# Kernel optimization log

Measured on AMD Instinct MI355X. Metric: run time of the kernel, lower is better.

The kernel has to match this reference:

```python
import jax, jax.numpy as jnp
import numpy as np

N_DIMS = 4          # len(dims): gauge-link channels split off by unpack_x
N_BANDS = 3         # SU(3) matrices
THRESHOLD = 1e-3    # trnorm_threshold
LAYER_CH = [6, 12, 12]  # input_channels + args.layer_channels


def cplx_einsum(eq, a, b):
    # complex einsum on real/imag-stacked tensors (last dim = 2)
    ar, ai = a[..., 0], a[..., 1]
    br, bi = b[..., 0], b[..., 1]
    re = jnp.einsum(eq, ar, br) - jnp.einsum(eq, ai, bi)
    im = jnp.einsum(eq, ar, bi) + jnp.einsum(eq, ai, br)
    return jnp.stack((re, im), axis=-1)


def h_conj(w):
    # hermitian conjugate: transpose matrix dims, negate imag part
    wt = jnp.swapaxes(w, -3, -2)
    return jnp.stack((wt[..., 0], -wt[..., 1]), axis=-1)


def gebl(x, weight):
    # x: [b, X, n_dims + n_in, nb, nb, 2]; weight: [n_out, w_in, w_in, 2]
    u, w = x[:, :, :N_DIMS], x[:, :, N_DIMS:]
    w = jnp.concatenate((w, h_conj(w)), axis=2)            # conjugation enlargement
    b, s = w.shape[0], w.shape[1]
    eye = jnp.zeros((N_BANDS, N_BANDS, 2), w.dtype).at[..., 0].set(jnp.eye(N_BANDS, dtype=w.dtype))
    unit = jnp.broadcast_to(eye, (b, s, 1, N_BANDS, N_BANDS, 2))
    w = jnp.concatenate((w, unit), axis=2)                 # unit elements
    ww = cplx_einsum('bxvij,bxwjk->bxvwik', w, w)          # pairwise matrix products
    w_out = cplx_einsum('uvw,bxvwij->bxuij', weight, ww)   # channel mixing
    return jnp.concatenate((u, w_out), axis=2)


def gerelu(x):
    u, w = x[:, :, :N_DIMS], x[:, :, N_DIMS:]
    tr_re = jnp.einsum('bxwiic->bxwc', w)[..., 0]          # Re(Tr W)
    w = jax.nn.relu(tr_re)[..., None, None, None] * w
    return jnp.concatenate((u, w), axis=2)


def trnorm(x):
    # trnorm_on_abs = True branch
    u, w = x[:, :, :N_DIMS], x[:, :, N_DIMS:]
    tr = jnp.einsum('bxviic->bxvc', w)
    tr_abs = jnp.sqrt(tr[..., 0] ** 2 + tr[..., 1] ** 2)
    norm = jnp.maximum(jnp.mean(tr_abs, axis=2), THRESHOLD)
    w = w / norm[:, :, None, None, None, None]
    return jnp.concatenate((u, w), axis=2)


def setup_inputs() -> dict:
    key = jax.random.key(0)
    ks = jax.random.split(key, 5)
    b, X = 2, 8 * 8 * 8 * 8
    x = jax.random.normal(ks[0], (b, X, N_DIMS + LAYER_CH[0], N_BANDS, N_BANDS, 2), jnp.float32)
    # GEBL weights: [n_out, w_in, w_in, 2], w_in = 2*n_in + 1
    w_in1 = 2 * LAYER_CH[0] + 1  # 13
    w_in2 = 2 * LAYER_CH[1] + 1  # 25
    w1 = jax.random.normal(ks[1], (LAYER_CH[1], w_in1, w_in1, 2), jnp.float32) * 0.1
    w2 = jax.random.normal(ks[2], (LAYER_CH[2], w_in2, w_in2, 2), jnp.float32) * 0.1
    dense_w = jax.random.normal(ks[3], (1, LAYER_CH[2] * 2), jnp.float32) * 0.2
    dense_b = jax.random.normal(ks[4], (1,), jnp.float32) * 0.01
    return {"x": x, "w1": w1, "w2": w2, "dense_w": dense_w, "dense_b": dense_b}


def reference(x, w1, w2, dense_w, dense_b):
    # GEBL -> GEReLU -> TrNorm (trnorm_before_ReLU=False), twice
    h = trnorm(gerelu(gebl(x, w1)))
    h = trnorm(gerelu(gebl(h, w2)))
    # Trace (normalized) -> reshape -> dense -> reshape
    w = h[:, :, N_DIMS:]
    tr = (1.0 / N_BANDS) * jnp.einsum('bxwiic->bxwc', w)   # [b, X, c, 2]
    flat = tr.reshape(-1, tr.shape[2] * 2)                 # torch .view: (c,2) interleaved
    out = flat @ dense_w.T + dense_b                        # [b*X, 1]
    return out.reshape(x.shape[0], -1)                      # [b, num_sites]
```

## Files before the change

### kernel.cpp

```cpp
#include <hip/hip_runtime.h>
#include <math.h>


#define NPTS 8192
#define THRESH 0.001f

__global__ void geblnet_setup(const float* __restrict__ w2,
                              float4* __restrict__ CTt) {
    int j = blockIdx.x * blockDim.x + threadIdx.x;
    if (j >= 12 * 169) return;
    int u = j / 169, it = j % 169;
    const float* W = w2 + u * 25 * 25 * 2;
#define WR(v, w) W[((v) * 25 + (w)) * 2]
#define WI(v, w) W[((v) * 25 + (w)) * 2 + 1]
    float c0, c1, c2, c3;
    if (it < 78) {
        int q = it, a = 0;
        while (q >= 12 - a) { q -= 12 - a; ++a; }
        int b = a + q;
        float ar = WR(a, b) + (a != b ? WR(b, a) : 0.f);
        float ai = WI(a, b) + (a != b ? WI(b, a) : 0.f);
        float br = WR(12 + a, 12 + b) + (a != b ? WR(12 + b, 12 + a) : 0.f);
        float bi = WI(12 + a, 12 + b) + (a != b ? WI(12 + b, 12 + a) : 0.f);
        c0 = ar + br; c1 = bi - ai; c2 = ai + bi; c3 = ar - br;
    } else if (it < 156) {
        int q = it - 78, a = 0;
        while (q >= 12 - a) { q -= 12 - a; ++a; }
        int b = a + q;
        if (a != b) {
            float gr = WR(a, 12 + b) + WR(12 + b, a);
            float gi = WI(a, 12 + b) + WI(12 + b, a);
            float dr = WR(b, 12 + a) + WR(12 + a, b);
            float di = WI(b, 12 + a) + WI(12 + a, b);
            c0 = gr + dr; c1 = di - gi; c2 = gi + di; c3 = gr - dr;
        } else {
            float er = WR(a, 12 + a) + WR(12 + a, a);
            float ei = WI(a, 12 + a) + WI(12 + a, a);
            c0 = er; c1 = 0.f; c2 = ei; c3 = 0.f;
        }
    } else if (it < 168) {
        int a = it - 156;
        float fr = WR(a, 24) + WR(24, a), fi = WI(a, 24) + WI(24, a);
        float pr = WR(12 + a, 24) + WR(24, 12 + a);
        float pi = WI(12 + a, 24) + WI(24, 12 + a);
        c0 = fr + pr; c1 = pi - fi; c2 = fi + pi; c3 = fr - pr;
    } else {
        c0 = 3.f * WR(24, 24); c1 = 0.f; c2 = 3.f * WI(24, 24); c3 = 0.f;
    }
    CTt[it * 12 + u] = make_float4(c0, c1, c2, c3);
#undef WR
#undef WI
}

union Scr {
    float2 bs[702];
    struct {
        float2 tpar[60];
        float2 tr1[12];
        float  sc1[12];
    } s;
};

__global__ __launch_bounds__(64) void geblnet_main(
    const float2* __restrict__ x2,
    const float2* __restrict__ w1g,
    const float* __restrict__ dw,
    const float* __restrict__ db,
    const float4* __restrict__ CTt,
    float* __restrict__ out)
{
    __shared__ float2 WeGV[170];
    __shared__ Scr S;
    __shared__ float2 Hs[108];

    const int t = threadIdx.x;
    const int p = blockIdx.x;

    for (int j = t; j < 117; j += 64) {
        int v = j / 9, ik = j - v * 9;
        int i = ik / 3, jj = ik - i * 3;
        float2 val;
        if (v < 6) val = x2[(size_t)p * 90 + (4 + v) * 9 + ik];
        else if (v < 12) {
            float2 s = x2[(size_t)p * 90 + (v - 2) * 9 + jj * 3 + i];
            val = make_float2(s.x, -s.y);
        } else val = make_float2((i == jj) ? 1.f : 0.f, 0.f);
        WeGV[v * 10 + ik] = val;
    }
    __syncthreads();

    #pragma unroll 1
    for (int g = 0; g < 2; ++g) {
        const int u0 = g * 6;
        #pragma unroll 1
        for (int j = t; j < 234; j += 64) {
            int row = j / 3;
            int d0 = (j - row * 3) * 3;
            int uu = row / 13;
            int v = row - uu * 13;
            const float2* cp = w1g + ((u0 + uu) * 13 + v) * 13;
            float ar0 = 0.f, ai0 = 0.f, ar1 = 0.f, ai1 = 0.f;
            float ar2 = 0.f, ai2 = 0.f;
            #pragma unroll
            for (int w = 0; w < 13; ++w) {
                float2 cc = cp[w];
                const float2* wr = &WeGV[w * 10 + d0];
                float2 e0 = wr[0], e1 = wr[1], e2 = wr[2];
                ar0 += cc.x * e0.x - cc.y * e0.y;
                ai0 += cc.x * e0.y + cc.y * e0.x;
                ar1 += cc.x * e1.x - cc.y * e1.y;
                ai1 += cc.x * e1.y + cc.y * e1.x;
                ar2 += cc.x * e2.x - cc.y * e2.y;
                ai2 += cc.x * e2.y + cc.y * e2.x;
            }
            float2* bp = &S.bs[(uu * 13 + v) * 9 + d0];
            bp[0] = make_float2(ar0, ai0);
            bp[1] = make_float2(ar1, ai1);
            bp[2] = make_float2(ar2, ai2);
        }
        __syncthreads();
        if (t < 54) {
            int uu = t / 9, ik = t - uu * 9;
            int i = ik / 3, k = ik - i * 3;
            float hr = 0.f, hi = 0.f;
            #pragma unroll
            for (int v = 0; v < 13; ++v) {
                const float2* a = &WeGV[v * 10 + i * 3];
                const float2* b = &S.bs[(uu * 13 + v) * 9 + k];
                #pragma unroll
                for (int j = 0; j < 3; ++j) {
                    float2 aj = a[j];
                    float2 bj = b[j * 3];
                    hr += aj.x * bj.x - aj.y * bj.y;
                    hi += aj.x * bj.y + aj.y * bj.x;
                }
            }
            Hs[(u0 + uu) * 9 + ik] = make_float2(hr, hi);
        }
        __syncthreads();
    }

    {
        float2 tt = make_float2(0.f, 0.f);
        float gg = 0.f, tra_v = 0.f;
        if (t < 12) {
            float2 a = Hs[t * 9 + 0], b = Hs[t * 9 + 4], c = Hs[t * 9 + 8];
            tt = make_float2(a.x + b.x + c.x, a.y + b.y + c.y);
            gg = tt.x > 0.f ? tt.x : 0.f;
            tra_v = gg * sqrtf(tt.x * tt.x + tt.y * tt.y);
        }
        float m = tra_v;
        m += __shfl_xor(m, 1, 16);
        m += __shfl_xor(m, 2, 16);
        m += __shfl_xor(m, 4, 16);
        m += __shfl_xor(m, 8, 16);
        if (t < 12) {
            S.s.tr1[t] = tt;
            S.s.sc1[t] = gg / fmaxf(m * (1.f / 12.f), THRESH);
        }
    }
    __syncthreads();

    const int q5 = t / 12, u5 = t - q5 * 12;
    const int i0 = q5 * 34;
    const bool act5 = (t < 60);
    const int pbase = act5 ? i0 * 12 + u5 : 0;
    float4 pc0 = CTt[pbase];
    float4 pc1 = CTt[pbase + 12];
    float4 pc2 = CTt[pbase + 24];
    float4 pc3 = CTt[pbase + 36];

    for (int it = t; it < 169; it += 64) {
        float2 val;
        if (it < 156) {
            int q = it < 78 ? it : it - 78;
            float fs = sqrtf(625.0f - 8.0f * (float)q);
            int a = (int)((25.0f - fs) * 0.5f);
            int b = q - (a * (25 - a)) / 2 + a;
            const float2* Ha = &Hs[a * 9];
            const float2* Hb = &Hs[b * 9];
            float s = S.s.sc1[a] * S.s.sc1[b];
            float vr = 0.f, vi = 0.f;
            if (it < 78) {
                #pragma unroll
                for (int i = 0; i < 3; ++i)
                    #pragma unroll
                    for (int jj = 0; jj < 3; ++jj) {
                        float2 A = Ha[i * 3 + jj], B = Hb[jj * 3 + i];
                        vr += A.x * B.x - A.y * B.y;
                        vi += A.x * B.y + A.y * B.x;
                    }
            } else {
                #pragma unroll
                for (int e = 0; e < 9; ++e) {
                    float2 A = Ha[e], B = Hb[e];
                    vr += A.x * B.x + A.y * B.y;
                    vi += A.y * B.x - A.x * B.y;
                }
            }
            val = make_float2(s * vr, s * vi);
        } else if (it < 168) {
            int a = it - 156;
            float s = S.s.sc1[a]; float2 tt = S.s.tr1[a];
            val = make_float2(s * tt.x, s * tt.y);
        } else {
            val = make_float2(1.f, 0.f);
        }
        WeGV[it] = val;
    }
    __syncthreads();

    if (act5) {
        const int i1 = (q5 == 4) ? 169 : i0 + 34;
        float2 g0 = WeGV[i0], g1 = WeGV[i0 + 1];
        float2 g2 = WeGV[i0 + 2], g3 = WeGV[i0 + 3];
        float tre = pc0.x * g0.x + pc0.y * g0.y
                  + pc1.x * g1.x + pc1.y * g1.y
                  + pc2.x * g2.x + pc2.y * g2.y
                  + pc3.x * g3.x + pc3.y * g3.y;
        float tim = pc0.z * g0.x + pc0.w * g0.y
                  + pc1.z * g1.x + pc1.w * g1.y
                  + pc2.z * g2.x + pc2.w * g2.y
                  + pc3.z * g3.x + pc3.w * g3.y;
        #pragma unroll 4
        for (int it = i0 + 4; it < i1; ++it) {
            float4 c = CTt[it * 12 + u5];
            float2 gv = WeGV[it];
            tre += c.x * gv.x + c.y * gv.y;
            tim += c.z * gv.x + c.w * gv.y;
        }
        S.s.tpar[u5 * 5 + q5] = make_float2(tre, tim);
    }
    __syncthreads();

    {
        float2 tt = make_float2(0.f, 0.f);
        float gg = 0.f, tra_v = 0.f;
        if (t < 12) {
            #pragma unroll
            for (int q = 0; q < 5; ++q) {
                float2 A = S.s.tpar[t * 5 + q];
                tt.x += A.x; tt.y += A.y;
            }
            gg = tt.x > 0.f ? tt.x : 0.f;
            tra_v = gg * sqrtf(tt.x * tt.x + tt.y * tt.y);
        }
        float m = tra_v;
        m += __shfl_xor(m, 1, 16);
        m += __shfl_xor(m, 2, 16);
        m += __shfl_xor(m, 4, 16);
        m += __shfl_xor(m, 8, 16);
        float term = 0.f;
        if (t < 12) {
            float inv = 1.f / fmaxf(m * (1.f / 12.f), THRESH);
            float s = gg * inv * (1.f / 3.f);
            term = s * (tt.x * dw[2 * t] + tt.y * dw[2 * t + 1]);
        }
        term += __shfl_xor(term, 1, 16);
        term += __shfl_xor(term, 2, 16);
        term += __shfl_xor(term, 4, 16);
        term += __shfl_xor(term, 8, 16);
        if (t == 0) out[p] = term + db[0];
    }
}

extern "C" void kernel_launch(void* const* d_in, const int* in_sizes, int n_in,
                              void* d_out, int out_size, void* d_ws, size_t ws_size,
                              hipStream_t stream) {
    const float* x  = (const float*)d_in[0];
    const float* w1 = (const float*)d_in[1];
    const float* w2 = (const float*)d_in[2];
    const float* dw = (const float*)d_in[3];
    const float* db = (const float*)d_in[4];
    float* outp = (float*)d_out;
    float4* CTt = (float4*)d_ws;

    geblnet_setup<<<(12 * 169 + 255) / 256, 256, 0, stream>>>(w2, CTt);

    geblnet_main<<<NPTS, 64, 0, stream>>>(
        (const float2*)x, (const float2*)w1, dw, db, CTt, outp);
}
```

Before: 125.4 us.

## Process two lattice sites per block to reuse weight loads

Each 64-thread block now handles two sites instead of one, so every w1 and CTt coefficient read from global memory feeds the arithmetic for both sites. The first mixing stage is remapped to one output element per thread instead of three, and the prefetch of the first CTt coefficients is dropped. Shared memory per block roughly doubles and the grid is halved, which lowers the number of waves but may reduce occupancy or latency hiding.

```diff
diff --git a/kernel.cpp b/kernel.cpp
--- a/kernel.cpp
+++ b/kernel.cpp
@@ -69,82 +69,100 @@
     const float4* __restrict__ CTt,
     float* __restrict__ out)
 {
-    __shared__ float2 WeGV[170];
-    __shared__ Scr S;
-    __shared__ float2 Hs[108];
+    __shared__ float2 WeGV_[2][170];
+    __shared__ Scr S_[2];
+    __shared__ float2 Hs_[2][108];
 
     const int t = threadIdx.x;
-    const int p = blockIdx.x;
+    const int pA = blockIdx.x * 2;
+    const int pB = pA + 1;
+
+    float2* WeA = WeGV_[0];
+    float2* WeB = WeGV_[1];
+    float2* HsA = Hs_[0];
+    float2* HsB = Hs_[1];
 
     for (int j = t; j < 117; j += 64) {
         int v = j / 9, ik = j - v * 9;
         int i = ik / 3, jj = ik - i * 3;
-        float2 val;
-        if (v < 6) val = x2[(size_t)p * 90 + (4 + v) * 9 + ik];
-        else if (v < 12) {
-            float2 s = x2[(size_t)p * 90 + (v - 2) * 9 + jj * 3 + i];
-            val = make_float2(s.x, -s.y);
-        } else val = make_float2((i == jj) ? 1.f : 0.f, 0.f);
-        WeGV[v * 10 + ik] = val;
+        float2 vaA, vaB;
+        if (v < 6) {
+            vaA = x2[(size_t)pA * 90 + (4 + v) * 9 + ik];
+            vaB = x2[(size_t)pB * 90 + (4 + v) * 9 + ik];
+        } else if (v < 12) {
+            float2 sA = x2[(size_t)pA * 90 + (v - 2) * 9 + jj * 3 + i];
+            float2 sB = x2[(size_t)pB * 90 + (v - 2) * 9 + jj * 3 + i];
+            vaA = make_float2(sA.x, -sA.y);
+            vaB = make_float2(sB.x, -sB.y);
+        } else {
+            vaA = make_float2((i == jj) ? 1.f : 0.f, 0.f);
+            vaB = vaA;
+        }
+        WeA[v * 10 + ik] = vaA;
+        WeB[v * 10 + ik] = vaB;
     }
     __syncthreads();
 
     #pragma unroll 1
     for (int g = 0; g < 2; ++g) {
         const int u0 = g * 6;
-        #pragma unroll 1
-        for (int j = t; j < 234; j += 64) {
-            int row = j / 3;
-            int d0 = (j - row * 3) * 3;
-            int uu = row / 13;
-            int v = row - uu * 13;
-            const float2* cp = w1g + ((u0 + uu) * 13 + v) * 13;
-            float ar0 = 0.f, ai0 = 0.f, ar1 = 0.f, ai1 = 0.f;
-            float ar2 = 0.f, ai2 = 0.f;
-            #pragma unroll
-            for (int w = 0; w < 13; ++w) {
-                float2 cc = cp[w];
-                const float2* wr = &WeGV[w * 10 + d0];
-                float2 e0 = wr[0], e1 = wr[1], e2 = wr[2];
-                ar0 += cc.x * e0.x - cc.y * e0.y;
-                ai0 += cc.x * e0.y + cc.y * e0.x;
-                ar1 += cc.x * e1.x - cc.y * e1.y;
-                ai1 += cc.x * e1.y + cc.y * e1.x;
-                ar2 += cc.x * e2.x - cc.y * e2.y;
-                ai2 += cc.x * e2.y + cc.y * e2.x;
+        {
+            int uu = 0, rem = t;
+            #pragma unroll 1
+            for (int e = t; e < 702; e += 64) {
+                int v = rem / 9, jk = rem - v * 9;
+                const float2* cp = w1g + ((u0 + uu) * 13 + v) * 13;
+                float brA = 0.f, biA = 0.f, brB = 0.f, biB = 0.f;
+                #pragma unroll
+                for (int w = 0; w < 13; ++w) {
+                    float2 cc = cp[w];
+                    float2 eA = WeA[w * 10 + jk];
+                    float2 eB = WeB[w * 10 + jk];
+                    brA += cc.x * eA.x - cc.y * eA.y;
+                    biA += cc.x * eA.y + cc.y * eA.x;
+                    brB += cc.x * eB.x - cc.y * eB.y;
+                    biB += cc.x * eB.y + cc.y * eB.x;
+                }
+                S_[0].bs[(uu * 13 + v) * 9 + jk] = make_float2(brA, biA);
+                S_[1].bs[(uu * 13 + v) * 9 + jk] = make_float2(brB, biB);
+                rem += 64;
+                if (rem >= 117) { rem -= 117; ++uu; }
             }
-            float2* bp = &S.bs[(uu * 13 + v) * 9 + d0];
-            bp[0] = make_float2(ar0, ai0);
-            bp[1] = make_float2(ar1, ai1);
-            bp[2] = make_float2(ar2, ai2);
         }
         __syncthreads();
         if (t < 54) {
             int uu = t / 9, ik = t - uu * 9;
             int i = ik / 3, k = ik - i * 3;
-            float hr = 0.f, hi = 0.f;
+            float hrA = 0.f, hiA = 0.f, hrB = 0.f, hiB = 0.f;
             #pragma unroll
             for (int v = 0; v < 13; ++v) {
-                const float2* a = &WeGV[v * 10 + i * 3];
-                const float2* b = &S.bs[(uu * 13 + v) * 9 + k];
+                const float2* aA = &WeA[v * 10 + i * 3];
+                const float2* aB = &WeB[v * 10 + i * 3];
+                const float2* bA = &S_[0].bs[(uu * 13 + v) * 9 + k];
+                const float2* bB = &S_[1].bs[(uu * 13 + v) * 9 + k];
                 #pragma unroll
                 for (int j = 0; j < 3; ++j) {
-                    float2 aj = a[j];
-                    float2 bj = b[j * 3];
-                    hr += aj.x * bj.x - aj.y * bj.y;
-                    hi += aj.x * bj.y + aj.y * bj.x;
+                    float2 ajA = aA[j], bjA = bA[j * 3];
+                    float2 ajB = aB[j], bjB = bB[j * 3];
+                    hrA += ajA.x * bjA.x - ajA.y * bjA.y;
+                    hiA += ajA.x * bjA.y + ajA.y * bjA.x;
+                    hrB += ajB.x * bjB.x - ajB.y * bjB.y;
+                    hiB += ajB.x * bjB.y + ajB.y * bjB.x;
                 }
             }
-            Hs[(u0 + uu) * 9 + ik] = make_float2(hr, hi);
+            HsA[(u0 + uu) * 9 + ik] = make_float2(hrA, hiA);
+            HsB[(u0 + uu) * 9 + ik] = make_float2(hrB, hiB);
         }
         __syncthreads();
     }
 
     {
+        const int grp = t >> 4, lu = t & 15;
         float2 tt = make_float2(0.f, 0.f);
         float gg = 0.f, tra_v = 0.f;
-        if (t < 12) {
-            float2 a = Hs[t * 9 + 0], b = Hs[t * 9 + 4], c = Hs[t * 9 + 8];
+        if (grp < 2 && lu < 12) {
+            const float2* H = (grp == 0) ? HsA : HsB;
+            float2 a = H[lu * 9 + 0], b = H[lu * 9 + 4], c = H[lu * 9 + 8];
             tt = make_float2(a.x + b.x + c.x, a.y + b.y + c.y);
             gg = tt.x > 0.f ? tt.x : 0.f;
             tra_v = gg * sqrtf(tt.x * tt.x + tt.y * tt.y);
@@ -154,92 +172,95 @@
         m += __shfl_xor(m, 2, 16);
         m += __shfl_xor(m, 4, 16);
         m += __shfl_xor(m, 8, 16);
-        if (t < 12) {
-            S.s.tr1[t] = tt;
-            S.s.sc1[t] = gg / fmaxf(m * (1.f / 12.f), THRESH);
+        if (grp < 2 && lu < 12) {
+            S_[grp].s.tr1[lu] = tt;
+            S_[grp].s.sc1[lu] = gg / fmaxf(m * (1.f / 12.f), THRESH);
         }
     }
     __syncthreads();
 
-    const int q5 = t / 12, u5 = t - q5 * 12;
-    const int i0 = q5 * 34;
-    const bool act5 = (t < 60);
-    const int pbase = act5 ? i0 * 12 + u5 : 0;
-    float4 pc0 = CTt[pbase];
-    float4 pc1 = CTt[pbase + 12];
-    float4 pc2 = CTt[pbase + 24];
-    float4 pc3 = CTt[pbase + 36];
-
     for (int it = t; it < 169; it += 64) {
-        float2 val;
+        float2 vA, vB;
         if (it < 156) {
             int q = it < 78 ? it : it - 78;
             float fs = sqrtf(625.0f - 8.0f * (float)q);
             int a = (int)((25.0f - fs) * 0.5f);
             int b = q - (a * (25 - a)) / 2 + a;
-            const float2* Ha = &Hs[a * 9];
-            const float2* Hb = &Hs[b * 9];
-            float s = S.s.sc1[a] * S.s.sc1[b];
-            float vr = 0.f, vi = 0.f;
+            const float2* HaA = &HsA[a * 9];
+            const float2* HbA = &HsA[b * 9];
+            const float2* HaB = &HsB[a * 9];
+            const float2* HbB = &HsB[b * 9];
+            float sA = S_[0].s.sc1[a] * S_[0].s.sc1[b];
+            float sB = S_[1].s.sc1[a] * S_[1].s.sc1[b];
+            float vrA = 0.f, viA = 0.f, vrB = 0.f, viB = 0.f;
             if (it < 78) {
                 #pragma unroll
                 for (int i = 0; i < 3; ++i)
                     #pragma unroll
                     for (int jj = 0; jj < 3; ++jj) {
-                        float2 A = Ha[i * 3 + jj], B = Hb[jj * 3 + i];
-                        vr += A.x * B.x - A.y * B.y;
-                        vi += A.x * B.y + A.y * B.x;
+                        float2 A = HaA[i * 3 + jj], B = HbA[jj * 3 + i];
+                        vrA += A.x * B.x - A.y * B.y;
+                        viA += A.x * B.y + A.y * B.x;
+                        float2 C = HaB[i * 3 + jj], D = HbB[jj * 3 + i];
+                        vrB += C.x * D.x - C.y * D.y;
+                        viB += C.x * D.y + C.y * D.x;
                     }
             } else {
                 #pragma unroll
                 for (int e = 0; e < 9; ++e) {
-                    float2 A = Ha[e], B = Hb[e];
-                    vr += A.x * B.x + A.y * B.y;
-                    vi += A.y * B.x - A.x * B.y;
+                    float2 A = HaA[e], B = HbA[e];
+                    vrA += A.x * B.x + A.y * B.y;
+                    viA += A.y * B.x - A.x * B.y;
+                    float2 C = HaB[e], D = HbB[e];
+                    vrB += C.x * D.x + C.y * D.y;
+                    viB += C.y * D.x - C.x * D.y;
                 }
             }
-            val = make_float2(s * vr, s * vi);
+            vA = make_float2(sA * vrA, sA * viA);
+            vB = make_float2(sB * vrB, sB * viB);
         } else if (it < 168) {
             int a = it - 156;
-            float s = S.s.sc1[a]; float2 tt = S.s.tr1[a];
-            val = make_float2(s * tt.x, s * tt.y);
+            float sA = S_[0].s.sc1[a]; float2 tA = S_[0].s.tr1[a];
+            float sB = S_[1].s.sc1[a]; float2 tB = S_[1].s.tr1[a];
+            vA = make_float2(sA * tA.x, sA * tA.y);
+            vB = make_float2(sB * tB.x, sB * tB.y);
         } else {
-            val = make_float2(1.f, 0.f);
-        }
-        WeGV[it] = val;
+            vA = make_float2(1.f, 0.f);
+            vB = vA;
+        }
+        WeA[it] = vA;
+        WeB[it] = vB;
     }
     __syncthreads();
 
-    if (act5) {
-        const int i1 = (q5 == 4) ? 169 : i0 + 34;
-        float2 g0 = WeGV[i0], g1 = WeGV[i0 + 1];
-        float2 g2 = WeGV[i0 + 2], g3 = WeGV[i0 + 3];
-        float tre = pc0.x * g0.x + pc0.y * g0.y
-                  + pc1.x * g1.x + pc1.y * g1.y
-                  + pc2.x * g2.x + pc2.y * g2.y
-                  + pc3.x * g3.x + pc3.y * g3.y;
-        float tim = pc0.z * g0.x + pc0.w * g0.y
-                  + pc1.z * g1.x + pc1.w * g1.y
-                  + pc2.z * g2.x + pc2.w * g2.y
-                  + pc3.z * g3.x + pc3.w * g3.y;
+    if (t < 60) {
+        int q = t / 12, u = t - q * 12;
+        int i0 = q * 34, i1 = (q == 4) ? 169 : i0 + 34;
+        float treA = 0.f, timA = 0.f, treB = 0.f, timB = 0.f;
         #pragma unroll 4
-        for (int it = i0 + 4; it < i1; ++it) {
-            float4 c = CTt[it * 12 + u5];
-            float2 gv = WeGV[it];
-            tre += c.x * gv.x + c.y * gv.y;
-            tim += c.z * gv.x + c.w * gv.y;
-        }
-        S.s.tpar[u5 * 5 + q5] = make_float2(tre, tim);
+        for (int it = i0; it < i1; ++it) {
+            float4 c = CTt[it * 12 + u];
+            float2 gA = WeA[it];
+            float2 gB = WeB[it];
+            treA += c.x * gA.x + c.y * gA.y;
+            timA += c.z * gA.x + c.w * gA.y;
+            treB += c.x * gB.x + c.y * gB.y;
+            timB += c.z * gB.x + c.w * gB.y;
+        }
+        S_[0].s.tpar[u * 5 + q] = make_float2(treA, timA);
+        S_[1].s.tpar[u * 5 + q] = make_float2(treB, timB);
     }
     __syncthreads();
 
     {
+        const int grp = t >> 4, lu = t & 15;
         float2 tt = make_float2(0.f, 0.f);
         float gg = 0.f, tra_v = 0.f;
-        if (t < 12) {
+        if (grp < 2 && lu < 12) {
+            const Scr* Sp = &S_[grp];
             #pragma unroll
             for (int q = 0; q < 5; ++q) {
-                float2 A = S.s.tpar[t * 5 + q];
+                float2 A = Sp->s.tpar[lu * 5 + q];
                 tt.x += A.x; tt.y += A.y;
             }
             gg = tt.x > 0.f ? tt.x : 0.f;
@@ -251,16 +272,16 @@
         m += __shfl_xor(m, 4, 16);
         m += __shfl_xor(m, 8, 16);
         float term = 0.f;
-        if (t < 12) {
+        if (grp < 2 && lu < 12) {
             float inv = 1.f / fmaxf(m * (1.f / 12.f), THRESH);
             float s = gg * inv * (1.f / 3.f);
-            term = s * (tt.x * dw[2 * t] + tt.y * dw[2 * t + 1]);
+            term = s * (tt.x * dw[2 * lu] + tt.y * dw[2 * lu + 1]);
         }
         term += __shfl_xor(term, 1, 16);
         term += __shfl_xor(term, 2, 16);
         term += __shfl_xor(term, 4, 16);
         term += __shfl_xor(term, 8, 16);
-        if (t == 0) out[p] = term + db[0];
+        if (grp < 2 && lu == 0) out[pA + grp] = term + db[0];
     }
 }
 
@@ -277,6 +298,6 @@
 
     geblnet_setup<<<(12 * 169 + 255) / 256, 256, 0, stream>>>(w2, CTt);
 
-    geblnet_main<<<NPTS, 64, 0, stream>>>(
+    geblnet_main<<<NPTS / 2, 64, 0, stream>>>(
         (const float2*)x, (const float2*)w1, dw, db, CTt, outp);
 }
```

Result: no change. 127.6 us (+1.8%).

## Restructure first GEBL stage with transposed shared layout and register-held operands

Applied to the files above, without the earlier changes.

Stores the enlarged input matrices transposed in shared memory with padded rows. Each of 63 lanes now caches its 13 input elements in registers and computes one output element per row, looping over the 78 channel rows in steps of 7. The weight rows are read from global memory and broadcast across the 9 lanes that share a row. The second contraction now reads contiguous padded vectors, and shared buffers are re-unioned to cut footprint. The CTt prefetch into registers before the second-layer trace is dropped. That may expose global load latency, and each weight load is now reused across fewer outputs per thread.

```diff
diff --git a/kernel.cpp b/kernel.cpp
--- a/kernel.cpp
+++ b/kernel.cpp
@@ -52,13 +52,17 @@
 #undef WI
 }
 
-union Scr {
-    float2 bs[702];
+union WeTU {
+    float2 weT[9 * 14];
     struct {
         float2 tpar[60];
         float2 tr1[12];
         float  sc1[12];
     } s;
+};
+union BsU {
+    float2 bs[6 * 9 * 14];
+    float2 gv[169];
 };
 
 __global__ __launch_bounds__(64) void geblnet_main(
@@ -69,9 +73,9 @@
     const float4* __restrict__ CTt,
     float* __restrict__ out)
 {
-    __shared__ float2 WeGV[170];
-    __shared__ Scr S;
-    __shared__ float2 Hs[108];
+    __shared__ __align__(16) WeTU W;
+    __shared__ __align__(16) BsU  B;
+    __shared__ __align__(16) float2 Hs[12 * 10];
 
     const int t = threadIdx.x;
     const int p = blockIdx.x;
@@ -85,38 +89,43 @@
             float2 s = x2[(size_t)p * 90 + (v - 2) * 9 + jj * 3 + i];
             val = make_float2(s.x, -s.y);
         } else val = make_float2((i == jj) ? 1.f : 0.f, 0.f);
-        WeGV[v * 10 + ik] = val;
-    }
-    __syncthreads();
+        W.weT[ik * 14 + v] = val;
+    }
+    __syncthreads();
+
+    const int rgrp = t / 9, jk = t - rgrp * 9;
+    const bool alane = (rgrp < 7);
+    float2 wc[13];
+    if (alane) {
+        #pragma unroll
+        for (int w = 0; w < 13; ++w) wc[w] = W.weT[jk * 14 + w];
+    }
 
     #pragma unroll 1
     for (int g = 0; g < 2; ++g) {
         const int u0 = g * 6;
-        #pragma unroll 1
-        for (int j = t; j < 234; j += 64) {
-            int row = j / 3;
-            int d0 = (j - row * 3) * 3;
-            int uu = row / 13;
-            int v = row - uu * 13;
-            const float2* cp = w1g + ((u0 + uu) * 13 + v) * 13;
-            float ar0 = 0.f, ai0 = 0.f, ar1 = 0.f, ai1 = 0.f;
-            float ar2 = 0.f, ai2 = 0.f;
-            #pragma unroll
-            for (int w = 0; w < 13; ++w) {
-                float2 cc = cp[w];
-                const float2* wr = &WeGV[w * 10 + d0];
-                float2 e0 = wr[0], e1 = wr[1], e2 = wr[2];
-                ar0 += cc.x * e0.x - cc.y * e0.y;
-                ai0 += cc.x * e0.y + cc.y * e0.x;
-                ar1 += cc.x * e1.x - cc.y * e1.y;
-                ai1 += cc.x * e1.y + cc.y * e1.x;
-                ar2 += cc.x * e2.x - cc.y * e2.y;
-                ai2 += cc.x * e2.y + cc.y * e2.x;
-            }
-            float2* bp = &S.bs[(uu * 13 + v) * 9 + d0];
-            bp[0] = make_float2(ar0, ai0);
-            bp[1] = make_float2(ar1, ai1);
-            bp[2] = make_float2(ar2, ai2);
+        if (alane) {
+            int row = rgrp;
+            int uu = 0, v = rgrp;
+            #pragma unroll 1
+            for (int b = 0; b < 12; ++b) {
+                int cu = uu, cv = v;
+                if (row >= 78) { cu = 0; cv = 0; }
+                const float2* cp = w1g + ((u0 + cu) * 13 + cv) * 13;
+                float br = 0.f, bi = 0.f;
+                #pragma unroll
+                for (int w = 0; w < 13; ++w) {
+                    float2 cc = cp[w];
+                    float2 ee = wc[w];
+                    br += cc.x * ee.x - cc.y * ee.y;
+                    bi += cc.x * ee.y + cc.y * ee.x;
+                }
+                if (row < 78)
+                    B.bs[(cu * 9 + jk) * 14 + cv] = make_float2(br, bi);
+                row += 7;
+                v += 7;
+                if (v >= 13) { v -= 13; ++uu; }
+            }
         }
         __syncthreads();
         if (t < 54) {
@@ -124,18 +133,17 @@
             int i = ik / 3, k = ik - i * 3;
             float hr = 0.f, hi = 0.f;
             #pragma unroll
-            for (int v = 0; v < 13; ++v) {
-                const float2* a = &WeGV[v * 10 + i * 3];
-                const float2* b = &S.bs[(uu * 13 + v) * 9 + k];
-                #pragma unroll
-                for (int j = 0; j < 3; ++j) {
-                    float2 aj = a[j];
-                    float2 bj = b[j * 3];
-                    hr += aj.x * bj.x - aj.y * bj.y;
-                    hi += aj.x * bj.y + aj.y * bj.x;
+            for (int j = 0; j < 3; ++j) {
+                const float2* wv = &W.weT[(i * 3 + j) * 14];
+                const float2* bv = &B.bs[(uu * 9 + j * 3 + k) * 14];
+                #pragma unroll
+                for (int v = 0; v < 13; ++v) {
+                    float2 a = wv[v], bb = bv[v];
+                    hr += a.x * bb.x - a.y * bb.y;
+                    hi += a.x * bb.y + a.y * bb.x;
                 }
             }
-            Hs[(u0 + uu) * 9 + ik] = make_float2(hr, hi);
+            Hs[(u0 + uu) * 10 + ik] = make_float2(hr, hi);
         }
         __syncthreads();
     }
@@ -144,7 +152,7 @@
         float2 tt = make_float2(0.f, 0.f);
         float gg = 0.f, tra_v = 0.f;
         if (t < 12) {
-            float2 a = Hs[t * 9 + 0], b = Hs[t * 9 + 4], c = Hs[t * 9 + 8];
+            float2 a = Hs[t * 10 + 0], b = Hs[t * 10 + 4], c = Hs[t * 10 + 8];
             tt = make_float2(a.x + b.x + c.x, a.y + b.y + c.y);
             gg = tt.x > 0.f ? tt.x : 0.f;
             tra_v = gg * sqrtf(tt.x * tt.x + tt.y * tt.y);
@@ -155,20 +163,11 @@
         m += __shfl_xor(m, 4, 16);
         m += __shfl_xor(m, 8, 16);
         if (t < 12) {
-            S.s.tr1[t] = tt;
-            S.s.sc1[t] = gg / fmaxf(m * (1.f / 12.f), THRESH);
-        }
-    }
-    __syncthreads();
-
-    const int q5 = t / 12, u5 = t - q5 * 12;
-    const int i0 = q5 * 34;
-    const bool act5 = (t < 60);
-    const int pbase = act5 ? i0 * 12 + u5 : 0;
-    float4 pc0 = CTt[pbase];
-    float4 pc1 = CTt[pbase + 12];
-    float4 pc2 = CTt[pbase + 24];
-    float4 pc3 = CTt[pbase + 36];
+            W.s.tr1[t] = tt;
+            W.s.sc1[t] = gg / fmaxf(m * (1.f / 12.f), THRESH);
+        }
+    }
+    __syncthreads();
 
     for (int it = t; it < 169; it += 64) {
         float2 val;
@@ -177,59 +176,51 @@
             float fs = sqrtf(625.0f - 8.0f * (float)q);
             int a = (int)((25.0f - fs) * 0.5f);
             int b = q - (a * (25 - a)) / 2 + a;
-            const float2* Ha = &Hs[a * 9];
-            const float2* Hb = &Hs[b * 9];
-            float s = S.s.sc1[a] * S.s.sc1[b];
+            const float2* Ha = &Hs[a * 10];
+            const float2* Hb = &Hs[b * 10];
+            float s = W.s.sc1[a] * W.s.sc1[b];
             float vr = 0.f, vi = 0.f;
             if (it < 78) {
                 #pragma unroll
                 for (int i = 0; i < 3; ++i)
                     #pragma unroll
                     for (int jj = 0; jj < 3; ++jj) {
-                        float2 A = Ha[i * 3 + jj], B = Hb[jj * 3 + i];
-                        vr += A.x * B.x - A.y * B.y;
-                        vi += A.x * B.y + A.y * B.x;
+                        float2 A = Ha[i * 3 + jj], Bb = Hb[jj * 3 + i];
+                        vr += A.x * Bb.x - A.y * Bb.y;
+                        vi += A.x * Bb.y + A.y * Bb.x;
                     }
             } else {
                 #pragma unroll
                 for (int e = 0; e < 9; ++e) {
-                    float2 A = Ha[e], B = Hb[e];
-                    vr += A.x * B.x + A.y * B.y;
-                    vi += A.y * B.x - A.x * B.y;
+                    float2 A = Ha[e], Bb = Hb[e];
+                    vr += A.x * Bb.x + A.y * Bb.y;
+                    vi += A.y * Bb.x - A.x * Bb.y;
                 }
             }
             val = make_float2(s * vr, s * vi);
         } else if (it < 168) {
             int a = it - 156;
-            float s = S.s.sc1[a]; float2 tt = S.s.tr1[a];
+            float s = W.s.sc1[a]; float2 tt = W.s.tr1[a];
             val = make_float2(s * tt.x, s * tt.y);
         } else {
             val = make_float2(1.f, 0.f);
         }
-        WeGV[it] = val;
-    }
-    __syncthreads();
-
-    if (act5) {
-        const int i1 = (q5 == 4) ? 169 : i0 + 34;
-        float2 g0 = WeGV[i0], g1 = WeGV[i0 + 1];
-        float2 g2 = WeGV[i0 + 2], g3 = WeGV[i0 + 3];
-        float tre = pc0.x * g0.x + pc0.y * g0.y
-                  + pc1.x * g1.x + pc1.y * g1.y
-                  + pc2.x * g2.x + pc2.y * g2.y
-                  + pc3.x * g3.x + pc3.y * g3.y;
-        float tim = pc0.z * g0.x + pc0.w * g0.y
-                  + pc1.z * g1.x + pc1.w * g1.y
-                  + pc2.z * g2.x + pc2.w * g2.y
-                  + pc3.z * g3.x + pc3.w * g3.y;
+        B.gv[it] = val;
+    }
+    __syncthreads();
+
+    if (t < 60) {
+        int q = t / 12, u = t - q * 12;
+        int i0 = q * 34, i1 = (q == 4) ? 169 : i0 + 34;
+        float tre = 0.f, tim = 0.f;
         #pragma unroll 4
-        for (int it = i0 + 4; it < i1; ++it) {
-            float4 c = CTt[it * 12 + u5];
-            float2 gv = WeGV[it];
+        for (int it = i0; it < i1; ++it) {
+            float4 c = CTt[it * 12 + u];
+            float2 gv = B.gv[it];
             tre += c.x * gv.x + c.y * gv.y;
             tim += c.z * gv.x + c.w * gv.y;
         }
-        S.s.tpar[u5 * 5 + q5] = make_float2(tre, tim);
+        W.s.tpar[u * 5 + q] = make_float2(tre, tim);
     }
     __syncthreads();
 
@@ -239,7 +230,7 @@
         if (t < 12) {
             #pragma unroll
             for (int q = 0; q < 5; ++q) {
-                float2 A = S.s.tpar[t * 5 + q];
+                float2 A = W.s.tpar[t * 5 + q];
                 tt.x += A.x; tt.y += A.y;
             }
             gg = tt.x > 0.f ? tt.x : 0.f;
```

Measured after the change: 129.0 us. 2.9% more time.

## Use packed FP32 FMA inline asm for complex MACs and remap first-layer work

Applied to the files above, without the earlier changes.

Replaces scalar complex multiply-accumulates with v_pk_fma_f32 inline-asm helpers (cmac, cmacc, cdot) and reorders the CTt coefficient layout to suit packed operands. The first-layer channel-mixing loop now gives each thread one output element over 702 items instead of three elements per thread. Input loading is restructured so each thread writes both a matrix and its conjugate transpose, and the register preloading of CTt coefficients before the second layer is removed. The aim is to halve FMA instruction count, at the cost of more loop iterations, reloading the same weights per element, and relying on op_sel/neg modifier semantics being correct.

```diff
diff --git a/kernel.cpp b/kernel.cpp
--- a/kernel.cpp
+++ b/kernel.cpp
@@ -4,6 +4,30 @@
 
 #define NPTS 8192
 #define THRESH 0.001f
+
+typedef float f32x2 __attribute__((ext_vector_type(2)));
+
+static __device__ __forceinline__ void cmac(f32x2& acc, f32x2 cc, f32x2 ee) {
+    asm("v_pk_fma_f32 %0, %1, %2, %0 op_sel:[0,0,0] op_sel_hi:[0,1,1]\n\t"
+        "v_pk_fma_f32 %0, %1, %2, %0 op_sel:[1,1,0] op_sel_hi:[1,0,1] neg_lo:[1,0,0]"
+        : "+v"(acc) : "v"(cc), "v"(ee));
+}
+
+static __device__ __forceinline__ void cmacc(f32x2& acc, f32x2 A, f32x2 B) {
+    asm("v_pk_fma_f32 %0, %1, %2, %0 op_sel:[0,0,0] op_sel_hi:[0,1,1] neg_hi:[1,0,0]\n\t"
+        "v_pk_fma_f32 %0, %1, %2, %0 op_sel:[1,1,0] op_sel_hi:[1,0,1]"
+        : "+v"(acc) : "v"(A), "v"(B));
+}
+
+static __device__ __forceinline__ void cdot(f32x2& acc, f32x2 gv, f32x2 cA, f32x2 cB) {
+    asm("v_pk_fma_f32 %0, %1, %2, %0 op_sel:[0,0,0] op_sel_hi:[0,1,1]\n\t"
+        "v_pk_fma_f32 %0, %1, %3, %0 op_sel:[1,0,0] op_sel_hi:[1,1,1]"
+        : "+v"(acc) : "v"(gv), "v"(cA), "v"(cB));
+}
+
+static __device__ __forceinline__ f32x2 c2(float2 a) {
+    f32x2 r; r.x = a.x; r.y = a.y; return r;
+}
 
 __global__ void geblnet_setup(const float* __restrict__ w2,
                               float4* __restrict__ CTt) {
@@ -13,7 +37,7 @@
     const float* W = w2 + u * 25 * 25 * 2;
 #define WR(v, w) W[((v) * 25 + (w)) * 2]
 #define WI(v, w) W[((v) * 25 + (w)) * 2 + 1]
-    float c0, c1, c2, c3;
+    float c0, c1, c2v, c3;
     if (it < 78) {
         int q = it, a = 0;
         while (q >= 12 - a) { q -= 12 - a; ++a; }
@@ -22,7 +46,7 @@
         float ai = WI(a, b) + (a != b ? WI(b, a) : 0.f);
         float br = WR(12 + a, 12 + b) + (a != b ? WR(12 + b, 12 + a) : 0.f);
         float bi = WI(12 + a, 12 + b) + (a != b ? WI(12 + b, 12 + a) : 0.f);
-        c0 = ar + br; c1 = bi - ai; c2 = ai + bi; c3 = ar - br;
+        c0 = ar + br; c1 = bi - ai; c2v = ai + bi; c3 = ar - br;
     } else if (it < 156) {
         int q = it - 78, a = 0;
         while (q >= 12 - a) { q -= 12 - a; ++a; }
@@ -32,22 +56,22 @@
             float gi = WI(a, 12 + b) + WI(12 + b, a);
             float dr = WR(b, 12 + a) + WR(12 + a, b);
             float di = WI(b, 12 + a) + WI(12 + a, b);
-            c0 = gr + dr; c1 = di - gi; c2 = gi + di; c3 = gr - dr;
+            c0 = gr + dr; c1 = di - gi; c2v = gi + di; c3 = gr - dr;
         } else {
             float er = WR(a, 12 + a) + WR(12 + a, a);
             float ei = WI(a, 12 + a) + WI(12 + a, a);
-            c0 = er; c1 = 0.f; c2 = ei; c3 = 0.f;
+            c0 = er; c1 = 0.f; c2v = ei; c3 = 0.f;
         }
     } else if (it < 168) {
         int a = it - 156;
         float fr = WR(a, 24) + WR(24, a), fi = WI(a, 24) + WI(24, a);
         float pr = WR(12 + a, 24) + WR(24, 12 + a);
         float pi = WI(12 + a, 24) + WI(24, 12 + a);
-        c0 = fr + pr; c1 = pi - fi; c2 = fi + pi; c3 = fr - pr;
+        c0 = fr + pr; c1 = pi - fi; c2v = fi + pi; c3 = fr - pr;
     } else {
-        c0 = 3.f * WR(24, 24); c1 = 0.f; c2 = 3.f * WI(24, 24); c3 = 0.f;
-    }
-    CTt[it * 12 + u] = make_float4(c0, c1, c2, c3);
+        c0 = 3.f * WR(24, 24); c1 = 0.f; c2v = 3.f * WI(24, 24); c3 = 0.f;
+    }
+    CTt[it * 12 + u] = make_float4(c0, c2v, c1, c3);
 #undef WR
 #undef WI
 }
@@ -76,66 +100,52 @@
     const int t = threadIdx.x;
     const int p = blockIdx.x;
 
-    for (int j = t; j < 117; j += 64) {
-        int v = j / 9, ik = j - v * 9;
-        int i = ik / 3, jj = ik - i * 3;
-        float2 val;
-        if (v < 6) val = x2[(size_t)p * 90 + (4 + v) * 9 + ik];
-        else if (v < 12) {
-            float2 s = x2[(size_t)p * 90 + (v - 2) * 9 + jj * 3 + i];
-            val = make_float2(s.x, -s.y);
-        } else val = make_float2((i == jj) ? 1.f : 0.f, 0.f);
-        WeGV[v * 10 + ik] = val;
+    if (t < 54) {
+        int xc = t / 9, ik = t - xc * 9;
+        int i = ik / 3, j = ik - i * 3;
+        float2 val = x2[(size_t)p * 90 + 36 + t];
+        WeGV[xc * 10 + ik] = val;
+        WeGV[(6 + xc) * 10 + j * 3 + i] = make_float2(val.x, -val.y);
+    } else if (t < 63) {
+        int ik = t - 54;
+        WeGV[120 + ik] = make_float2((ik % 4 == 0) ? 1.f : 0.f, 0.f);
     }
     __syncthreads();
 
     #pragma unroll 1
     for (int g = 0; g < 2; ++g) {
         const int u0 = g * 6;
-        #pragma unroll 1
-        for (int j = t; j < 234; j += 64) {
-            int row = j / 3;
-            int d0 = (j - row * 3) * 3;
-            int uu = row / 13;
-            int v = row - uu * 13;
-            const float2* cp = w1g + ((u0 + uu) * 13 + v) * 13;
-            float ar0 = 0.f, ai0 = 0.f, ar1 = 0.f, ai1 = 0.f;
-            float ar2 = 0.f, ai2 = 0.f;
-            #pragma unroll
-            for (int w = 0; w < 13; ++w) {
-                float2 cc = cp[w];
-                const float2* wr = &WeGV[w * 10 + d0];
-                float2 e0 = wr[0], e1 = wr[1], e2 = wr[2];
-                ar0 += cc.x * e0.x - cc.y * e0.y;
-                ai0 += cc.x * e0.y + cc.y * e0.x;
-                ar1 += cc.x * e1.x - cc.y * e1.y;
-                ai1 += cc.x * e1.y + cc.y * e1.x;
-                ar2 += cc.x * e2.x - cc.y * e2.y;
-                ai2 += cc.x * e2.y + cc.y * e2.x;
-            }
-            float2* bp = &S.bs[(uu * 13 + v) * 9 + d0];
-            bp[0] = make_float2(ar0, ai0);
-            bp[1] = make_float2(ar1, ai1);
-            bp[2] = make_float2(ar2, ai2);
+        {
+            int uu = 0, rem = t;
+            #pragma unroll 2
+            for (int e = t; e < 702; e += 64) {
+                int v = rem / 9, jk = rem - v * 9;
+                const float2* cp = w1g + ((u0 + uu) * 13 + v) * 13;
+                f32x2 acc = {0.f, 0.f};
+                #pragma unroll
+                for (int w = 0; w < 13; ++w) {
+                    cmac(acc, c2(cp[w]), c2(WeGV[w * 10 + jk]));
+                }
+                S.bs[(uu * 13 + v) * 9 + jk] = make_float2(acc.x, acc.y);
+                rem += 64;
+                if (rem >= 117) { rem -= 117; ++uu; }
+            }
         }
         __syncthreads();
         if (t < 54) {
             int uu = t / 9, ik = t - uu * 9;
             int i = ik / 3, k = ik - i * 3;
-            float hr = 0.f, hi = 0.f;
+            f32x2 h = {0.f, 0.f};
             #pragma unroll
             for (int v = 0; v < 13; ++v) {
                 const float2* a = &WeGV[v * 10 + i * 3];
                 const float2* b = &S.bs[(uu * 13 + v) * 9 + k];
                 #pragma unroll
                 for (int j = 0; j < 3; ++j) {
-                    float2 aj = a[j];
-                    float2 bj = b[j * 3];
-                    hr += aj.x * bj.x - aj.y * bj.y;
-                    hi += aj.x * bj.y + aj.y * bj.x;
+                    cmac(h, c2(a[j]), c2(b[j * 3]));
                 }
             }
-            Hs[(u0 + uu) * 9 + ik] = make_float2(hr, hi);
+            Hs[(u0 + uu) * 9 + ik] = make_float2(h.x, h.y);
         }
         __syncthreads();
     }
@@ -160,15 +170,6 @@
         }
     }
     __syncthreads();
-
-    const int q5 = t / 12, u5 = t - q5 * 12;
-    const int i0 = q5 * 34;
-    const bool act5 = (t < 60);
-    const int pbase = act5 ? i0 * 12 + u5 : 0;
-    float4 pc0 = CTt[pbase];
-    float4 pc1 = CTt[pbase + 12];
-    float4 pc2 = CTt[pbase + 24];
-    float4 pc3 = CTt[pbase + 36];
 
     for (int it = t; it < 169; it += 64) {
         float2 val;
@@ -180,25 +181,19 @@
             const float2* Ha = &Hs[a * 9];
             const float2* Hb = &Hs[b * 9];
             float s = S.s.sc1[a] * S.s.sc1[b];
-            float vr = 0.f, vi = 0.f;
+            f32x2 vv = {0.f, 0.f};
             if (it < 78) {
                 #pragma unroll
                 for (int i = 0; i < 3; ++i)
                     #pragma unroll
-                    for (int jj = 0; jj < 3; ++jj) {
-                        float2 A = Ha[i * 3 + jj], B = Hb[jj * 3 + i];
-                        vr += A.x * B.x - A.y * B.y;
-                        vi += A.x * B.y + A.y * B.x;
-                    }
+                    for (int jj = 0; jj < 3; ++jj)
+                        cmac(vv, c2(Ha[i * 3 + jj]), c2(Hb[jj * 3 + i]));
             } else {
                 #pragma unroll
-                for (int e = 0; e < 9; ++e) {
-                    float2 A = Ha[e], B = Hb[e];
-                    vr += A.x * B.x + A.y * B.y;
-                    vi += A.y * B.x - A.x * B.y;
-                }
-            }
-            val = make_float2(s * vr, s * vi);
+                for (int e = 0; e < 9; ++e)
+                    cmacc(vv, c2(Ha[e]), c2(Hb[e]));
+            }
+            val = make_float2(s * vv.x, s * vv.y);
         } else if (it < 168) {
             int a = it - 156;
             float s = S.s.sc1[a]; float2 tt = S.s.tr1[a];
@@ -210,26 +205,18 @@
     }
     __syncthreads();
 
-    if (act5) {
-        const int i1 = (q5 == 4) ? 169 : i0 + 34;
-        float2 g0 = WeGV[i0], g1 = WeGV[i0 + 1];
-        float2 g2 = WeGV[i0 + 2], g3 = WeGV[i0 + 3];
-        float tre = pc0.x * g0.x + pc0.y * g0.y
-                  + pc1.x * g1.x + pc1.y * g1.y
-                  + pc2.x * g2.x + pc2.y * g2.y
-                  + pc3.x * g3.x + pc3.y * g3.y;
-        float tim = pc0.z * g0.x + pc0.w * g0.y
-                  + pc1.z * g1.x + pc1.w * g1.y
-                  + pc2.z * g2.x + pc2.w * g2.y
-                  + pc3.z * g3.x + pc3.w * g3.y;
+    if (t < 60) {
+        int q = t / 12, u = t - q * 12;
+        int i0 = q * 34, i1 = (q == 4) ? 169 : i0 + 34;
+        f32x2 acc = {0.f, 0.f};
         #pragma unroll 4
-        for (int it = i0 + 4; it < i1; ++it) {
-            float4 c = CTt[it * 12 + u5];
-            float2 gv = WeGV[it];
-            tre += c.x * gv.x + c.y * gv.y;
-            tim += c.z * gv.x + c.w * gv.y;
-        }
-        S.s.tpar[u5 * 5 + q5] = make_float2(tre, tim);
+        for (int it = i0; it < i1; ++it) {
+            float4 c = CTt[it * 12 + u];
+            f32x2 cA; cA.x = c.x; cA.y = c.y;
+            f32x2 cB; cB.x = c.z; cB.y = c.w;
+            cdot(acc, c2(WeGV[it]), cA, cB);
+        }
+        S.s.tpar[u * 5 + q] = make_float2(acc.x, acc.y);
     }
     __syncthreads();
 
```

Measured after the change: 121.8 us. 1.03x faster.
